# Kernel optimization log

Hardware: AMD Instinct MI355X
Metric: run time of the kernel (lower is better)

## Reference

```python
import jax, jax.numpy as jnp
import numpy as np

EPS = 1e-5


def spline_conv(x, src, dst, pseudo, W, root, bias, num_nodes, K=5):
    """Degree-1 open B-spline conv (torch_spline_conv semantics), mean aggregation.
    W: [kernel_total, Cin, Cout]. kernel_total==1 means trivial basis (kernel_size=1)."""
    E = src.shape[0]
    Cin = x.shape[1]
    KT = W.shape[0]
    x_j = x[src]                                            # [E, Cin] edge gather
    deg = jax.ops.segment_sum(jnp.ones((E,), x.dtype), dst, num_segments=num_nodes)
    deg = jnp.maximum(deg, 1.0)
    if KT == 1:
        agg = jax.ops.segment_sum(x_j, dst, num_segments=num_nodes)
        out = (agg / deg[:, None]) @ W[0]
    else:
        v = pseudo * (K - 1)                                # open spline: v in [0, K-1]
        f = jnp.clip(jnp.floor(v), 0.0, K - 2)
        frac = v - f                                        # [E, 2]
        fi = f.astype(jnp.int32)
        # bucket basis-weighted source features by (kernel_index, dst) then one dense einsum
        h = jnp.zeros((KT * num_nodes, Cin), x.dtype)
        for s0 in (0, 1):
            for s1 in (0, 1):
                b0 = frac[:, 0] if s0 else 1.0 - frac[:, 0]
                b1 = frac[:, 1] if s1 else 1.0 - frac[:, 1]
                basis = b0 * b1                             # [E]
                wi = (fi[:, 0] + s0) + K * (fi[:, 1] + s1)  # [E] kernel index in [0,25)
                seg = wi * num_nodes + dst
                h = h + jax.ops.segment_sum(basis[:, None] * x_j, seg,
                                            num_segments=KT * num_nodes)
        agg = jnp.einsum('knc,kco->no', h.reshape(KT, num_nodes, Cin), W)
        out = agg / deg[:, None]
    return out + x @ root + bias


def batch_norm(x, gamma, beta):
    m = x.mean(axis=0)
    var = jnp.mean((x - m) ** 2, axis=0)
    return gamma * (x - m) * jax.lax.rsqrt(var + EPS) + beta


def setup_inputs() -> dict:
    key = jax.random.key(0)
    ks = jax.random.split(key, 8)
    N, E, Cin, Cout = 50000, 800000, 32, 64
    x = jax.random.normal(ks[0], (N, Cin), jnp.float32)
    edge_index = jax.random.randint(ks[1], (2, E), 0, N, jnp.int32)
    edge_attr = jax.random.uniform(ks[2], (E, 2), jnp.float32)
    s = 0.1
    return {
        'x': x, 'edge_index': edge_index, 'edge_attr': edge_attr,
        'w1': jax.random.normal(ks[3], (25, Cin, Cout), jnp.float32) * s,
        'r1': jax.random.normal(ks[4], (Cin, Cout), jnp.float32) * s,
        'b1': jnp.zeros((Cout,), jnp.float32),
        'g1': jnp.ones((Cout,), jnp.float32),
        'beta1': jnp.zeros((Cout,), jnp.float32),
        'w2': jax.random.normal(ks[5], (25, Cout, Cout), jnp.float32) * s,
        'r2': jax.random.normal(ks[6], (Cout, Cout), jnp.float32) * s,
        'b2': jnp.zeros((Cout,), jnp.float32),
        'g2': jnp.ones((Cout,), jnp.float32),
        'beta2': jnp.zeros((Cout,), jnp.float32),
        'ws': jax.random.normal(ks[7], (1, Cin, Cout), jnp.float32) * s,
        'rs': jax.random.normal(jax.random.fold_in(key, 99), (Cin, Cout), jnp.float32) * s,
        'bs': jnp.zeros((Cout,), jnp.float32),
        'gs': jnp.ones((Cout,), jnp.float32),
        'betas': jnp.zeros((Cout,), jnp.float32),
    }


def reference(x, edge_index, edge_attr, w1, r1, b1, g1, beta1,
              w2, r2, b2, g2, beta2, ws, rs, bs, gs, betas):
    N = x.shape[0]
    src, dst = edge_index[0], edge_index[1]
    h = jax.nn.elu(batch_norm(spline_conv(x, src, dst, edge_attr, w1, r1, b1, N), g1, beta1))
    left = batch_norm(spline_conv(h, src, dst, edge_attr, w2, r2, b2, N), g2, beta2)
    short = batch_norm(spline_conv(x, src, dst, edge_attr, ws, rs, bs, N), gs, betas)
    return jax.nn.elu(left + short)
```

## Files before the change

kernel.cpp:

```cpp
#include <hip/hip_runtime.h>

#define NN 50000
#define NE 800000
#define DBINS 1024

typedef __attribute__((ext_vector_type(8))) short bf16x8;
typedef __attribute__((ext_vector_type(4))) float f32x4;

__device__ __forceinline__ unsigned short f2bf(float f) {
    union { float f; unsigned u; } v; v.f = f;
    unsigned r = v.u + 0x7FFFu + ((v.u >> 16) & 1u);
    return (unsigned short)(r >> 16);
}

__device__ __forceinline__ int us_idx(int kk, int r, int m) {
    return kk*544 + (r >> 3)*136 + m*8 + (r & 7);
}

template<int CIN, int NT>
__device__ __forceinline__ void stage1_node(
        const int* __restrict__ epsrc,
        const unsigned short* __restrict__ wfull,
        const unsigned short* __restrict__ Xh,
        int ebeg, int degp, int lane,
        f32x4 (&d)[2][NT]) {
#pragma unroll
    for (int mt = 0; mt < 2; ++mt)
#pragma unroll
        for (int nt = 0; nt < NT; ++nt)
            d[mt][nt] = f32x4{0.f, 0.f, 0.f, 0.f};
    if (degp <= 0) return;
    const int l15 = lane & 15;
    const int kb = (lane >> 4) * 8;
    const int last = degp - 1;
    for (int k0 = 0; k0 < degp; k0 += 32) {
        int e[8]; int s[8]; bool val[8];
#pragma unroll
        for (int j = 0; j < 8; ++j) {
            int k = k0 + kb + j;
            val[j] = (k < degp);
            e[j] = ebeg + min(k, last);
        }
#pragma unroll
        for (int j = 0; j < 8; ++j) s[j] = epsrc[e[j]];
        union { unsigned short us[8]; bf16x8 v; } a0, a1;
#pragma unroll
        for (int j = 0; j < 8; ++j) {
            unsigned short w0 = wfull[(size_t)e[j]*32 + l15];
            unsigned short w1 = wfull[(size_t)e[j]*32 + 16 + l15];
            a0.us[j] = val[j] ? w0 : (unsigned short)0;
            a1.us[j] = val[j] ? w1 : (unsigned short)0;
        }
#pragma unroll
        for (int nt = 0; nt < NT; ++nt) {
            union { unsigned short us[8]; bf16x8 v; } b;
#pragma unroll
            for (int j = 0; j < 8; ++j)
                b.us[j] = Xh[(size_t)s[j]*CIN + nt*16 + l15];
            d[0][nt] = __builtin_amdgcn_mfma_f32_16x16x32_bf16(a0.v, b.v, d[0][nt], 0, 0, 0);
            d[1][nt] = __builtin_amdgcn_mfma_f32_16x16x32_bf16(a1.v, b.v, d[1][nt], 0, 0, 0);
        }
    }
}

__global__ __launch_bounds__(256) void k_zero(int* degi, int* cur, float* stats,
                                              int* dcnt, int* dcur,
                                              unsigned* xz, unsigned* hz) {
    int i = blockIdx.x*256 + threadIdx.x;
    int stride = gridDim.x*256;
    for (int j = i; j < NN; j += stride) { degi[j] = 0; cur[j] = 0; }
    if (i < 384) stats[i] = 0.f;
    if (i < DBINS) { dcnt[i] = 0; dcur[i] = 0; }
    if (i < 16) xz[i] = 0u;
    if (i < 32) hz[i] = 0u;
}

__global__ __launch_bounds__(256) void k_hist(const int* __restrict__ dst, int* degi) {
    int e = blockIdx.x*256 + threadIdx.x;
    if (e < NE) atomicAdd(&degi[dst[e]], 1);
}

__global__ __launch_bounds__(256) void k_scan_block(const int* __restrict__ degi,
                                                    int* off, int* bsum) {
    __shared__ int sh[256];
    int t = threadIdx.x;
    int base = blockIdx.x * 1024;
    int v[4]; int s = 0;
#pragma unroll
    for (int j = 0; j < 4; j++) {
        int idx = base + t*4 + j;
        v[j] = (idx < NN) ? ((degi[idx] + 3) & ~3) : 0;
        s += v[j];
    }
    sh[t] = s; __syncthreads();
    for (int ofs = 1; ofs < 256; ofs <<= 1) {
        int x = (t >= ofs) ? sh[t - ofs] : 0;
        __syncthreads();
        sh[t] += x;
        __syncthreads();
    }
    int ex = sh[t] - s;
#pragma unroll
    for (int j = 0; j < 4; j++) {
        int idx = base + t*4 + j;
        if (idx < NN) off[idx] = ex;
        ex += v[j];
    }
    if (t == 255) bsum[blockIdx.x] = sh[255];
}

__global__ __launch_bounds__(256) void k_dhist(const int* __restrict__ degi, int* dcnt) {
    __shared__ int lh[DBINS];
    int t = threadIdx.x;
#pragma unroll
    for (int j = 0; j < DBINS/256; ++j) lh[t + 256*j] = 0;
    __syncthreads();
    int n = blockIdx.x*256 + t;
    if (n < NN) atomicAdd(&lh[min(degi[n], DBINS-1)], 1);
    __syncthreads();
#pragma unroll
    for (int j = 0; j < DBINS/256; ++j) {
        int b = t + 256*j;
        if (lh[b]) atomicAdd(&dcnt[b], lh[b]);
    }
}

__global__ __launch_bounds__(256) void k_topscan(const int* __restrict__ bsum,
                                                 int* bpre, int nb,
                                                 const int* __restrict__ dcnt,
                                                 int* dbase) {
    __shared__ int sh[256];
    int t = threadIdx.x;
    if (blockIdx.x == 0) {
        int s = (t < nb) ? bsum[t] : 0;
        sh[t] = s; __syncthreads();
        for (int ofs = 1; ofs < 256; ofs <<= 1) {
            int x = (t >= ofs) ? sh[t - ofs] : 0;
            __syncthreads();
            sh[t] += x;
            __syncthreads();
        }
        if (t < nb) bpre[t] = sh[t] - s;
    } else {
        int v[4]; int s = 0;
#pragma unroll
        for (int j = 0; j < 4; j++) { v[j] = dcnt[t*4 + j]; s += v[j]; }
        sh[t] = s; __syncthreads();
        for (int ofs = 1; ofs < 256; ofs <<= 1) {
            int x = (t >= ofs) ? sh[t - ofs] : 0;
            __syncthreads();
            sh[t] += x;
            __syncthreads();
        }
        int ex = sh[t] - s;
#pragma unroll
        for (int j = 0; j < 4; j++) { dbase[t*4 + j] = ex; ex += v[j]; }
    }
}

__global__ __launch_bounds__(256) void k_scan_add(int* off, const int* __restrict__ bpre,
                                                  const int* __restrict__ degi) {
    int i = blockIdx.x*256 + threadIdx.x;
    if (i < NN) {
        int v = off[i] + bpre[i >> 10];
        off[i] = v;
        if (i == NN - 1) off[NN] = v + ((degi[i] + 3) & ~3);
    }
}

__global__ __launch_bounds__(256) void k_pscatter_pad(const int* __restrict__ degi,
                                                      const int* __restrict__ dbase,
                                                      int* dcur, int* perm,
                                                      const int* __restrict__ off,
                                                      int* __restrict__ epsrc,
                                                      unsigned short* __restrict__ wfull) {
    __shared__ int lh[DBINS];
    __shared__ int lb[DBINS];
    int t = threadIdx.x;
#pragma unroll
    for (int j = 0; j < DBINS/256; ++j) lh[t + 256*j] = 0;
    __syncthreads();
    int n = blockIdx.x*256 + t;
    int d = 0, lr = 0;
    bool act = (n < NN);
    if (act) {
        d = min(degi[n], DBINS-1);
        lr = atomicAdd(&lh[d], 1);
    }
    __syncthreads();
#pragma unroll
    for (int j = 0; j < DBINS/256; ++j) {
        int b = t + 256*j;
        int c = lh[b];
        lb[b] = c ? atomicAdd(&dcur[b], c) : 0;
    }
    __syncthreads();
    if (act) {
        perm[dbase[d] + lb[d] + lr] = n;
        int base = off[n] + degi[n];
        int end  = off[n + 1];
        uint4 z = make_uint4(0u, 0u, 0u, 0u);
        for (int p = base; p < end; ++p) {
            epsrc[p] = NN;
            uint4* wp = (uint4*)(wfull + (size_t)p * 32);
            wp[0] = z; wp[1] = z; wp[2] = z; wp[3] = z;
        }
    }
}

__global__ __launch_bounds__(256) void k_scatter(const int* __restrict__ src,
                                                 const int* __restrict__ dst,
                                                 const float* __restrict__ ea,
                                                 const int* __restrict__ off, int* cur,
                                                 int* __restrict__ epsrc,
                                                 unsigned short* __restrict__ wfull) {
    int e = blockIdx.x*256 + threadIdx.x;
    if (e >= NE) return;
    int d = dst[e];
    int p = off[d] + atomicAdd(&cur[d], 1);
    float v0 = ea[2*e]     * 4.f;
    float v1 = ea[2*e + 1] * 4.f;
    float wx[5], wy[5];
#pragma unroll
    for (int r = 0; r < 5; ++r) {
        wx[r] = fmaxf(1.f - fabsf(v0 - (float)r), 0.f);
        wy[r] = fmaxf(1.f - fabsf(v1 - (float)r), 0.f);
    }
    union { unsigned short s[32]; uint4 q[4]; } u;
#pragma unroll
    for (int r1 = 0; r1 < 5; ++r1)
#pragma unroll
        for (int r0 = 0; r0 < 5; ++r0)
            u.s[r1*5 + r0] = f2bf(wx[r0] * wy[r1]);
    u.s[25] = 0x3F80;
#pragma unroll
    for (int i = 26; i < 32; ++i) u.s[i] = 0;
    epsrc[p] = src[e];
    uint4* wp = (uint4*)(wfull + (size_t)p * 32);
    wp[0] = u.q[0]; wp[1] = u.q[1]; wp[2] = u.q[2]; wp[3] = u.q[3];
}

__device__ __forceinline__ void wprep_body(int tid, const float* W, const float* root,
                                           int KTC, unsigned short* Wb) {
    int lane = tid & 63, cot = (tid >> 6) & 3, kk = tid >> 8;
    int co = 16*cot + (lane & 15);
    int kbase = kk*32 + ((lane >> 4) * 8);
    union { unsigned short s[8]; uint4 v; } u;
#pragma unroll
    for (int j = 0; j < 8; j++) {
        int k = kbase + j;
        float val = (k < KTC) ? W[(size_t)k*64 + co] : root[(size_t)(k - KTC)*64 + co];
        u.s[j] = f2bf(val);
    }
    *(uint4*)(Wb + (size_t)tid * 8) = u.v;
}

__global__ __launch_bounds__(256) void k_prep(const float* __restrict__ x,
                                              unsigned short* __restrict__ xb,
                                              const float* __restrict__ w1,
                                              const float* __restrict__ r1,
                                              unsigned short* Wb1,
                                              const float* __restrict__ wsN,
                                              const float* __restrict__ rs,
                                              unsigned short* WbS,
                                              const float* __restrict__ w2,
                                              const float* __restrict__ r2,
                                              unsigned short* Wb2) {
    int b = blockIdx.x, t = threadIdx.x;
    if (b < 1563) {
        int i = b*256 + t;
        if (i >= NN*8) return;
        float4 v = ((const float4*)x)[i];
        uint2 pk;
        pk.x = (unsigned)f2bf(v.x) | ((unsigned)f2bf(v.y) << 16);
        pk.y = (unsigned)f2bf(v.z) | ((unsigned)f2bf(v.w) << 16);
        ((uint2*)xb)[i] = pk;
    } else if (b < 1589) {
        wprep_body((b - 1563)*256 + t, w1, r1, 800, Wb1);
    } else if (b < 1591) {
        wprep_body((b - 1589)*256 + t, wsN, rs, 32, WbS);
    } else {
        wprep_body((b - 1591)*256 + t, w2, r2, 1600, Wb2);
    }
}

__global__ __launch_bounds__(512, 6) void k_conv1s(
        const unsigned short* __restrict__ Xh,
        const int* __restrict__ off,
        const int* __restrict__ degi,
        const int* __restrict__ epsrc,
        const unsigned short* __restrict__ wfull,
        const int* __restrict__ perm,
        const unsigned short* __restrict__ Wb1,
        const unsigned short* __restrict__ WbS,
        const float* __restrict__ b1,
        const float* __restrict__ bs,
        float* __restrict__ agg1,
        float* __restrict__ aggS) {
    __shared__ __align__(16) unsigned short hb[28*544];
    unsigned* hb32 = (unsigned*)hb;
    const int t = threadIdx.x, lane = t & 63, w = t >> 6;
    const int n0 = NN - 16 - blockIdx.x * 16;
    const int l15 = lane & 15;
    const int wib = (lane >> 4) * 4;

#pragma unroll
    for (int nn = 0; nn < 2; ++nn) {
        const int g = 2*w + nn;
        const int n = perm[n0 + g];
        const int deg = degi[n];
        const int degp = (deg + 3) & ~3;
        f32x4 d[2][2];
        stage1_node<32, 2>(epsrc, wfull, Xh, off[n], degp, lane, d);
        const float rdeg = 1.f / (float)max(deg, 1);
        const int basel = (l15 >> 3)*136 + g*8 + (l15 & 7);
#pragma unroll
        for (int mt = 0; mt < 2; ++mt)
#pragma unroll
            for (int nt = 0; nt < 2; ++nt)
#pragma unroll
                for (int r = 0; r < 4; ++r) {
                    int wi = mt*16 + wib + r;
                    if (wi <= 25) {
                        int kk = (wi < 25) ? wi : 26;
                        hb[kk*544 + nt*272 + basel] = f2bf(d[mt][nt][r] * rdeg);
                    }
                }
    }
    if ((lane & 31) < 16) {
        const int g2 = 2*w + (lane >> 5);
        const int cd = lane & 15;
        const int n2 = perm[n0 + g2];
        unsigned xv = ((const unsigned*)Xh)[(size_t)n2*16 + cd];
        const int r0 = 2*cd;
        const int dwb = (r0 >> 3)*68 + g2*4 + ((r0 & 7) >> 1);
        hb32[25*272 + dwb] = xv;
        hb32[27*272 + dwb] = xv;
    }
    __syncthreads();

    const int m = l15, qq = lane >> 4;
    const int co = (w & 3)*16 + m;
    const int4 pn = ((const int4*)perm)[(n0 >> 2) + qq];
    const int prow[4] = {pn.x, pn.y, pn.z, pn.w};
    if (w < 4) {
        f32x4 acc = {0.f, 0.f, 0.f, 0.f};
        for (int kk = 0; kk < 26; ++kk) {
            bf16x8 av = *(const bf16x8*)&hb[kk*544 + qq*136 + m*8];
            bf16x8 bv = *(const bf16x8*)(Wb1 + (size_t)((kk*4 + w)*64 + lane) * 8);
            acc = __builtin_amdgcn_mfma_f32_16x16x32_bf16(av, bv, acc, 0, 0, 0);
        }
        const float bb = b1[co];
#pragma unroll
        for (int r = 0; r < 4; ++r)
            agg1[(size_t)prow[r]*64 + co] = acc[r] + bb;
    } else {
        f32x4 accs = {0.f, 0.f, 0.f, 0.f};
#pragma unroll
        for (int s = 0; s < 2; ++s) {
            bf16x8 av = *(const bf16x8*)&hb[(26 + s)*544 + qq*136 + m*8];
            bf16x8 bv = *(const bf16x8*)(WbS + (size_t)((s*4 + (w & 3))*64 + lane) * 8);
            accs = __builtin_amdgcn_mfma_f32_16x16x32_bf16(av, bv, accs, 0, 0, 0);
        }
        const float bb = bs[co];
#pragma unroll
        for (int r = 0; r < 4; ++r)
            aggS[(size_t)prow[r]*64 + co] = accs[r] + bb;
    }
}

__global__ __launch_bounds__(512, 4) void k_conv2(
        const unsigned short* __restrict__ Xh,
        const int* __restrict__ off,
        const int* __restrict__ degi,
        const int* __restrict__ epsrc,
        const unsigned short* __restrict__ wfull,
        const int* __restrict__ perm,
        const unsigned short* __restrict__ Wb2,
        const float* __restrict__ b2,
        float* __restrict__ agg) {
    __shared__ __align__(16) unsigned short hb[52*544];
    unsigned* hb32 = (unsigned*)hb;
    const int t = threadIdx.x, lane = t & 63, w = t >> 6;
    const int n0 = NN - 16 - blockIdx.x * 16;
    const int l15 = lane & 15;
    const int wib = (lane >> 4) * 4;

#pragma unroll
    for (int nn = 0; nn < 2; ++nn) {
        const int g = 2*w + nn;
        const int n = perm[n0 + g];
        const int deg = degi[n];
        const int degp = (deg + 3) & ~3;
        f32x4 d[2][4];
        stage1_node<64, 4>(epsrc, wfull, Xh, off[n], degp, lane, d);
        const float rdeg = 1.f / (float)max(deg, 1);
        const int basel = (l15 >> 3)*136 + g*8 + (l15 & 7);
#pragma unroll
        for (int mt = 0; mt < 2; ++mt)
#pragma unroll
            for (int nt = 0; nt < 4; ++nt) {
                const int cadd = (nt >> 1)*544 + (nt & 1)*272 + basel;
#pragma unroll
                for (int r = 0; r < 4; ++r) {
                    int wi = mt*16 + wib + r;
                    if (wi < 25)
                        hb[wi*1088 + cadd] = f2bf(d[mt][nt][r] * rdeg);
                }
            }
    }
    {
        const int g2 = 2*w + (lane >> 5);
        const int c2 = lane & 31;
        const int n2 = perm[n0 + g2];
        unsigned xv = ((const unsigned*)Xh)[(size_t)n2*32 + c2];
        const int r0 = (2*c2) & 31;
        const int dw = (50 + (c2 >> 4))*272 + (r0 >> 3)*68 + g2*4 + ((r0 & 7) >> 1);
        hb32[dw] = xv;
    }
    __syncthreads();

    if (w >= 4) return;
    const int m = l15, qq = lane >> 4;
    f32x4 acc = {0.f, 0.f, 0.f, 0.f};
    for (int kk = 0; kk < 52; ++kk) {
        bf16x8 av = *(const bf16x8*)&hb[kk*544 + qq*136 + m*8];
        bf16x8 bv = *(const bf16x8*)(Wb2 + (size_t)((kk*4 + w)*64 + lane) * 8);
        acc = __builtin_amdgcn_mfma_f32_16x16x32_bf16(av, bv, acc, 0, 0, 0);
    }
    const int4 pn = ((const int4*)perm)[(n0 >> 2) + qq];
    const int prow[4] = {pn.x, pn.y, pn.z, pn.w};
    const int co = w*16 + m;
    const float bb = b2[co];
#pragma unroll
    for (int rr = 0; rr < 4; ++rr)
        agg[(size_t)prow[rr]*64 + co] = acc[rr] + bb;
}

__global__ __launch_bounds__(256) void k_bnstats(const float* __restrict__ agg, float* stats) {
    __shared__ float sh0[256], sh1[256];
    int t = threadIdx.x;
    float s = 0.f, ss = 0.f;
    int stride = gridDim.x * 256;
    for (int i = blockIdx.x*256 + t; i < NN*64; i += stride) {
        float v = agg[i];
        s += v; ss += v*v;
    }
    sh0[t] = s; sh1[t] = ss;
    __syncthreads();
    if (t < 64) {
        float a = sh0[t] + sh0[t+64] + sh0[t+128] + sh0[t+192];
        float b = sh1[t] + sh1[t+64] + sh1[t+128] + sh1[t+192];
        atomicAdd(&stats[t], a);
        atomicAdd(&stats[64 + t], b);
    }
}

__global__ __launch_bounds__(256) void k_bnstats2(const float* __restrict__ a1,
                                                  const float* __restrict__ as,
                                                  float* stats) {
    __shared__ float sh0[256], sh1[256];
    int t = threadIdx.x;
    const float* src = (blockIdx.x < 256) ? a1 : as;
    float* dst = (blockIdx.x < 256) ? (stats + 128) : (stats + 256);
    int bid = (blockIdx.x < 256) ? blockIdx.x : blockIdx.x - 256;
    float s = 0.f, ss = 0.f;
    for (int i = bid*256 + t; i < NN*64; i += 256*256) {
        float v = src[i];
        s += v; ss += v*v;
    }
    sh0[t] = s; sh1[t] = ss;
    __syncthreads();
    if (t < 64) {
        float a = sh0[t] + sh0[t+64] + sh0[t+128] + sh0[t+192];
        float b = sh1[t] + sh1[t+64] + sh1[t+128] + sh1[t+192];
        atomicAdd(&dst[t], a);
        atomicAdd(&dst[64 + t], b);
    }
}

__device__ __forceinline__ float eluf(float u) { return u > 0.f ? u : expm1f(u); }

__global__ __launch_bounds__(256) void k_bn_elu(const float* __restrict__ agg,
                                                const float* __restrict__ stats,
                                                const float* __restrict__ gamma,
                                                const float* __restrict__ beta,
                                                unsigned short* __restrict__ outb) {
    int i = blockIdx.x*256 + threadIdx.x;
    if (i >= NN*16) return;
    float4 v = ((const float4*)agg)[i];
    float r[4] = {v.x, v.y, v.z, v.w};
    int c0 = (i << 2) & 63;
#pragma unroll
    for (int j = 0; j < 4; j++) {
        int c = c0 + j;
        float mu = stats[c] * (1.f/NN);
        float var = stats[64 + c] * (1.f/NN) - mu*mu;
        float sc = gamma[c] * rsqrtf(fmaxf(var, 0.f) + 1e-5f);
        r[j] = eluf((r[j] - mu)*sc + beta[c]);
    }
    uint2 pk;
    pk.x = (unsigned)f2bf(r[0]) | ((unsigned)f2bf(r[1]) << 16);
    pk.y = (unsigned)f2bf(r[2]) | ((unsigned)f2bf(r[3]) << 16);
    ((uint2*)outb)[i] = pk;
}

__global__ __launch_bounds__(256) void k_bn_final(const float* __restrict__ a2,
                                                  const float* __restrict__ st2,
                                                  const float* __restrict__ g2,
                                                  const float* __restrict__ be2,
                                                  const float* __restrict__ as,
                                                  const float* __restrict__ sts,
                                                  const float* __restrict__ gs,
                                                  const float* __restrict__ bes,
                                                  float* __restrict__ out) {
    int i = blockIdx.x*256 + threadIdx.x;
    if (i >= NN*16) return;
    float4 v2 = ((const float4*)a2)[i];
    float4 vs = ((const float4*)as)[i];
    float r2v[4] = {v2.x, v2.y, v2.z, v2.w};
    float rsv[4] = {vs.x, vs.y, vs.z, vs.w};
    float o[4];
    int c0 = (i << 2) & 63;
#pragma unroll
    for (int j = 0; j < 4; j++) {
        int c = c0 + j;
        float mu2 = st2[c] * (1.f/NN);
        float var2 = st2[64 + c] * (1.f/NN) - mu2*mu2;
        float sc2 = g2[c] * rsqrtf(fmaxf(var2, 0.f) + 1e-5f);
        float mus = sts[c] * (1.f/NN);
        float vars = sts[64 + c] * (1.f/NN) - mus*mus;
        float scs = gs[c] * rsqrtf(fmaxf(vars, 0.f) + 1e-5f);
        float u = (r2v[j] - mu2)*sc2 + be2[c] + (rsv[j] - mus)*scs + bes[c];
        o[j] = eluf(u);
    }
    ((float4*)out)[i] = make_float4(o[0], o[1], o[2], o[3]);
}

extern "C" void kernel_launch(void* const* d_in, const int* in_sizes, int n_in,
                              void* d_out, int out_size, void* d_ws, size_t ws_size,
                              hipStream_t stream) {
    const float* x   = (const float*)d_in[0];
    const int*   ei  = (const int*)d_in[1];
    const float* ea  = (const float*)d_in[2];
    const float* w1  = (const float*)d_in[3];
    const float* r1  = (const float*)d_in[4];
    const float* b1  = (const float*)d_in[5];
    const float* g1  = (const float*)d_in[6];
    const float* be1 = (const float*)d_in[7];
    const float* w2  = (const float*)d_in[8];
    const float* r2  = (const float*)d_in[9];
    const float* b2  = (const float*)d_in[10];
    const float* g2  = (const float*)d_in[11];
    const float* be2 = (const float*)d_in[12];
    const float* wsN = (const float*)d_in[13];
    const float* rs  = (const float*)d_in[14];
    const float* bs  = (const float*)d_in[15];
    const float* gs  = (const float*)d_in[16];
    const float* bes = (const float*)d_in[17];
    const int* srcp = ei;
    const int* dstp = ei + NE;

    char* wsb = (char*)d_ws;
    size_t o = 0;
    auto alloc = [&](size_t bytes) -> char* {
        char* p = wsb + o;
        o += (bytes + 255) & ~(size_t)255;
        return p;
    };
    int*    degi    = (int*)   alloc((size_t)NN * 4);
    int*    cur     = (int*)   alloc((size_t)NN * 4);
    int*    off     = (int*)   alloc((size_t)(NN + 1) * 4);
    int*    bsum    = (int*)   alloc(256 * 4);
    int*    bpre    = (int*)   alloc(256 * 4);
    int*    dcnt    = (int*)   alloc(DBINS * 4);
    int*    dcur    = (int*)   alloc(DBINS * 4);
    int*    dbase   = (int*)   alloc(DBINS * 4);
    int*    perm    = (int*)   alloc((size_t)NN * 4);
    int*    epsrc   = (int*)   alloc(((size_t)NE + 3*NN + 64) * 4);
    unsigned short* wfull = (unsigned short*)alloc(((size_t)NE + 3*NN + 64) * 64);
    unsigned short* Wb1 = (unsigned short*)alloc(26 * 4096);
    unsigned short* WbS = (unsigned short*)alloc(2 * 4096);
    unsigned short* Wb2 = (unsigned short*)alloc(52 * 4096);
    float*  agg1    = (float*) alloc((size_t)NN * 64 * 4);
    float*  aggS    = (float*) alloc((size_t)NN * 64 * 4);
    unsigned short* h1bf = (unsigned short*)alloc((size_t)(NN + 1) * 64 * 2);
    unsigned short* xbf  = (unsigned short*)alloc((size_t)(NN + 1) * 32 * 2);
    float*  stats   = (float*) alloc(384 * 4);
    (void)ws_size; (void)in_sizes; (void)n_in; (void)out_size;

    float* out = (float*)d_out;

    k_zero<<<196, 256, 0, stream>>>(degi, cur, stats, dcnt, dcur,
                                    (unsigned*)(xbf + (size_t)NN * 32),
                                    (unsigned*)(h1bf + (size_t)NN * 64));
    k_hist<<<3125, 256, 0, stream>>>(dstp, degi);
    k_scan_block<<<49, 256, 0, stream>>>(degi, off, bsum);
    k_dhist<<<196, 256, 0, stream>>>(degi, dcnt);
    k_topscan<<<2, 256, 0, stream>>>(bsum, bpre, 49, dcnt, dbase);
    k_scan_add<<<196, 256, 0, stream>>>(off, bpre, degi);
    k_pscatter_pad<<<196, 256, 0, stream>>>(degi, dbase, dcur, perm, off, epsrc, wfull);
    k_scatter<<<3125, 256, 0, stream>>>(srcp, dstp, ea, off, cur, epsrc, wfull);

    k_prep<<<1643, 256, 0, stream>>>(x, xbf, w1, r1, Wb1, wsN, rs, WbS, w2, r2, Wb2);

    k_conv1s<<<3125, 512, 0, stream>>>(xbf, off, degi, epsrc, wfull, perm,
                                       Wb1, WbS, b1, bs, agg1, aggS);
    k_bnstats<<<256, 256, 0, stream>>>(agg1, stats);
    k_bn_elu<<<3125, 256, 0, stream>>>(agg1, stats, g1, be1, h1bf);

    k_conv2<<<3125, 512, 0, stream>>>(h1bf, off, degi, epsrc, wfull, perm,
                                      Wb2, b2, agg1);
    k_bnstats2<<<512, 256, 0, stream>>>(agg1, aggS, stats);
    k_bn_final<<<3125, 256, 0, stream>>>(agg1, stats + 128, g2, be2,
                                         aggS, stats + 256, gs, bes, out);
}
```

Measured before the change: 431.5 us.

## Store compact per-edge records and recompute spline basis inside conv via 32x32 MFMA

Replaces the per-edge 64-byte precomputed bf16 basis vector plus separate src array with one 16-byte record (src, scaled pseudo coords). The conv kernels now recompute each lane's basis weight on the fly. The stage-1 gather-matmul switches from paired 16x16x32 MFMAs to a single 32x32x16 MFMA per column tile, with the epilogue remapped to match. This cuts scatter write traffic and the edge-data reads in both convs, at the cost of extra ALU work per edge and lower occupancy (launch bounds 6 to 5).

```diff
diff --git a/kernel.cpp b/kernel.cpp
--- a/kernel.cpp
+++ b/kernel.cpp
@@ -6,6 +6,7 @@
 
 typedef __attribute__((ext_vector_type(8))) short bf16x8;
 typedef __attribute__((ext_vector_type(4))) float f32x4;
+typedef __attribute__((ext_vector_type(16))) float f32x16;
 
 __device__ __forceinline__ unsigned short f2bf(float f) {
     union { float f; unsigned u; } v; v.f = f;
@@ -13,52 +14,50 @@
     return (unsigned short)(r >> 16);
 }
 
+__device__ __forceinline__ int4 ld_ep1(const int4* ep, unsigned idx) {
+    return *(const int4*)((const char*)ep + (size_t)(idx * 16u));
+}
+
 __device__ __forceinline__ int us_idx(int kk, int r, int m) {
     return kk*544 + (r >> 3)*136 + m*8 + (r & 7);
 }
 
-template<int CIN, int NT>
-__device__ __forceinline__ void stage1_node(
-        const int* __restrict__ epsrc,
-        const unsigned short* __restrict__ wfull,
+template<int CIN, int NT2>
+__device__ __forceinline__ void stage1_node32(
+        const int4* __restrict__ ep,
         const unsigned short* __restrict__ Xh,
         int ebeg, int degp, int lane,
-        f32x4 (&d)[2][NT]) {
-#pragma unroll
-    for (int mt = 0; mt < 2; ++mt)
-#pragma unroll
-        for (int nt = 0; nt < NT; ++nt)
-            d[mt][nt] = f32x4{0.f, 0.f, 0.f, 0.f};
+        float r0, float r1, int wsel,
+        f32x16 (&d)[NT2]) {
+#pragma unroll
+    for (int nt = 0; nt < NT2; ++nt)
+#pragma unroll
+        for (int r = 0; r < 16; ++r) d[nt][r] = 0.f;
     if (degp <= 0) return;
-    const int l15 = lane & 15;
-    const int kb = (lane >> 4) * 8;
+    const int m = lane & 31;
+    const int kb = (lane >> 5) * 8;
     const int last = degp - 1;
-    for (int k0 = 0; k0 < degp; k0 += 32) {
-        int e[8]; int s[8]; bool val[8];
+    for (int k0 = 0; k0 < degp; k0 += 16) {
+        int s[8];
+        union { unsigned short us[8]; bf16x8 v; } a;
 #pragma unroll
         for (int j = 0; j < 8; ++j) {
             int k = k0 + kb + j;
-            val[j] = (k < degp);
-            e[j] = ebeg + min(k, last);
-        }
-#pragma unroll
-        for (int j = 0; j < 8; ++j) s[j] = epsrc[e[j]];
-        union { unsigned short us[8]; bf16x8 v; } a0, a1;
-#pragma unroll
-        for (int j = 0; j < 8; ++j) {
-            unsigned short w0 = wfull[(size_t)e[j]*32 + l15];
-            unsigned short w1 = wfull[(size_t)e[j]*32 + 16 + l15];
-            a0.us[j] = val[j] ? w0 : (unsigned short)0;
-            a1.us[j] = val[j] ? w1 : (unsigned short)0;
-        }
-#pragma unroll
-        for (int nt = 0; nt < NT; ++nt) {
+            int4 P = ld_ep1(ep, (unsigned)(ebeg + min(k, last)));
+            s[j] = P.x;
+            float v0 = __int_as_float(P.y), v1 = __int_as_float(P.z);
+            float wxa = fmaxf(1.f - fabsf(v0 - r0), 0.f);
+            float wya = fmaxf(1.f - fabsf(v1 - r1), 0.f);
+            float wv = (wsel == 0) ? wxa * wya : ((wsel == 1) ? 1.f : 0.f);
+            a.us[j] = (k < degp) ? f2bf(wv) : (unsigned short)0;
+        }
+#pragma unroll
+        for (int nt = 0; nt < NT2; ++nt) {
             union { unsigned short us[8]; bf16x8 v; } b;
 #pragma unroll
             for (int j = 0; j < 8; ++j)
-                b.us[j] = Xh[(size_t)s[j]*CIN + nt*16 + l15];
-            d[0][nt] = __builtin_amdgcn_mfma_f32_16x16x32_bf16(a0.v, b.v, d[0][nt], 0, 0, 0);
-            d[1][nt] = __builtin_amdgcn_mfma_f32_16x16x32_bf16(a1.v, b.v, d[1][nt], 0, 0, 0);
+                b.us[j] = Xh[(size_t)s[j]*CIN + nt*32 + m];
+            d[nt] = __builtin_amdgcn_mfma_f32_32x32x16_bf16(a.v, b.v, d[nt], 0, 0, 0);
         }
     }
 }
@@ -172,8 +171,7 @@
                                                       const int* __restrict__ dbase,
                                                       int* dcur, int* perm,
                                                       const int* __restrict__ off,
-                                                      int* __restrict__ epsrc,
-                                                      unsigned short* __restrict__ wfull) {
+                                                      int4* __restrict__ ep) {
     __shared__ int lh[DBINS];
     __shared__ int lb[DBINS];
     int t = threadIdx.x;
@@ -199,12 +197,8 @@
         perm[dbase[d] + lb[d] + lr] = n;
         int base = off[n] + degi[n];
         int end  = off[n + 1];
-        uint4 z = make_uint4(0u, 0u, 0u, 0u);
-        for (int p = base; p < end; ++p) {
-            epsrc[p] = NN;
-            uint4* wp = (uint4*)(wfull + (size_t)p * 32);
-            wp[0] = z; wp[1] = z; wp[2] = z; wp[3] = z;
-        }
+        for (int p = base; p < end; ++p)
+            ep[p] = make_int4(NN, __float_as_int(1e9f), __float_as_int(1e9f), 0);
     }
 }
 
@@ -212,32 +206,14 @@
                                                  const int* __restrict__ dst,
                                                  const float* __restrict__ ea,
                                                  const int* __restrict__ off, int* cur,
-                                                 int* __restrict__ epsrc,
-                                                 unsigned short* __restrict__ wfull) {
+                                                 int4* __restrict__ ep) {
     int e = blockIdx.x*256 + threadIdx.x;
     if (e >= NE) return;
     int d = dst[e];
     int p = off[d] + atomicAdd(&cur[d], 1);
     float v0 = ea[2*e]     * 4.f;
     float v1 = ea[2*e + 1] * 4.f;
-    float wx[5], wy[5];
-#pragma unroll
-    for (int r = 0; r < 5; ++r) {
-        wx[r] = fmaxf(1.f - fabsf(v0 - (float)r), 0.f);
-        wy[r] = fmaxf(1.f - fabsf(v1 - (float)r), 0.f);
-    }
-    union { unsigned short s[32]; uint4 q[4]; } u;
-#pragma unroll
-    for (int r1 = 0; r1 < 5; ++r1)
-#pragma unroll
-        for (int r0 = 0; r0 < 5; ++r0)
-            u.s[r1*5 + r0] = f2bf(wx[r0] * wy[r1]);
-    u.s[25] = 0x3F80;
-#pragma unroll
-    for (int i = 26; i < 32; ++i) u.s[i] = 0;
-    epsrc[p] = src[e];
-    uint4* wp = (uint4*)(wfull + (size_t)p * 32);
-    wp[0] = u.q[0]; wp[1] = u.q[1]; wp[2] = u.q[2]; wp[3] = u.q[3];
+    ep[p] = make_int4(src[e], __float_as_int(v0), __float_as_int(v1), 0);
 }
 
 __device__ __forceinline__ void wprep_body(int tid, const float* W, const float* root,
@@ -284,12 +260,11 @@
     }
 }
 
-__global__ __launch_bounds__(512, 6) void k_conv1s(
+__global__ __launch_bounds__(512, 5) void k_conv1s(
         const unsigned short* __restrict__ Xh,
         const int* __restrict__ off,
         const int* __restrict__ degi,
-        const int* __restrict__ epsrc,
-        const unsigned short* __restrict__ wfull,
+        const int4* __restrict__ ep,
         const int* __restrict__ perm,
         const unsigned short* __restrict__ Wb1,
         const unsigned short* __restrict__ WbS,
@@ -301,8 +276,11 @@
     unsigned* hb32 = (unsigned*)hb;
     const int t = threadIdx.x, lane = t & 63, w = t >> 6;
     const int n0 = NN - 16 - blockIdx.x * 16;
-    const int l15 = lane & 15;
-    const int wib = (lane >> 4) * 4;
+    const int m32 = lane & 31;
+    const int hh = lane >> 5;
+    const float r0 = (float)(m32 % 5), r1 = (float)(m32 / 5);
+    const int wsel = (m32 < 25) ? 0 : ((m32 == 25) ? 1 : 2);
+    const int basel = (m32 >> 3)*136 + (m32 & 7);
 
 #pragma unroll
     for (int nn = 0; nn < 2; ++nn) {
@@ -310,36 +288,31 @@
         const int n = perm[n0 + g];
         const int deg = degi[n];
         const int degp = (deg + 3) & ~3;
-        f32x4 d[2][2];
-        stage1_node<32, 2>(epsrc, wfull, Xh, off[n], degp, lane, d);
+        f32x16 d[1];
+        stage1_node32<32, 1>(ep, Xh, off[n], degp, lane, r0, r1, wsel, d);
         const float rdeg = 1.f / (float)max(deg, 1);
-        const int basel = (l15 >> 3)*136 + g*8 + (l15 & 7);
-#pragma unroll
-        for (int mt = 0; mt < 2; ++mt)
-#pragma unroll
-            for (int nt = 0; nt < 2; ++nt)
-#pragma unroll
-                for (int r = 0; r < 4; ++r) {
-                    int wi = mt*16 + wib + r;
-                    if (wi <= 25) {
-                        int kk = (wi < 25) ? wi : 26;
-                        hb[kk*544 + nt*272 + basel] = f2bf(d[mt][nt][r] * rdeg);
-                    }
-                }
+#pragma unroll
+        for (int reg = 0; reg < 16; ++reg) {
+            int wi = (reg & 3) + 8*(reg >> 2) + 4*hh;
+            if (wi <= 25) {
+                int kk = (wi < 25) ? wi : 26;
+                hb[kk*544 + basel + g*8] = f2bf(d[0][reg] * rdeg);
+            }
+        }
     }
     if ((lane & 31) < 16) {
-        const int g2 = 2*w + (lane >> 5);
+        const int g2 = 2*w + hh;
         const int cd = lane & 15;
         const int n2 = perm[n0 + g2];
         unsigned xv = ((const unsigned*)Xh)[(size_t)n2*16 + cd];
-        const int r0 = 2*cd;
-        const int dwb = (r0 >> 3)*68 + g2*4 + ((r0 & 7) >> 1);
+        const int r0d = 2*cd;
+        const int dwb = (r0d >> 3)*68 + g2*4 + ((r0d & 7) >> 1);
         hb32[25*272 + dwb] = xv;
         hb32[27*272 + dwb] = xv;
     }
     __syncthreads();
 
-    const int m = l15, qq = lane >> 4;
+    const int m = lane & 15, qq = lane >> 4;
     const int co = (w & 3)*16 + m;
     const int4 pn = ((const int4*)perm)[(n0 >> 2) + qq];
     const int prow[4] = {pn.x, pn.y, pn.z, pn.w};
@@ -373,8 +346,7 @@
         const unsigned short* __restrict__ Xh,
         const int* __restrict__ off,
         const int* __restrict__ degi,
-        const int* __restrict__ epsrc,
-        const unsigned short* __restrict__ wfull,
+        const int4* __restrict__ ep,
         const int* __restrict__ perm,
         const unsigned short* __restrict__ Wb2,
         const float* __restrict__ b2,
@@ -383,8 +355,11 @@
     unsigned* hb32 = (unsigned*)hb;
     const int t = threadIdx.x, lane = t & 63, w = t >> 6;
     const int n0 = NN - 16 - blockIdx.x * 16;
-    const int l15 = lane & 15;
-    const int wib = (lane >> 4) * 4;
+    const int m32 = lane & 31;
+    const int hh = lane >> 5;
+    const float r0 = (float)(m32 % 5), r1 = (float)(m32 / 5);
+    const int wsel = (m32 < 25) ? 0 : ((m32 == 25) ? 1 : 2);
+    const int basel = (m32 >> 3)*136 + (m32 & 7);
 
 #pragma unroll
     for (int nn = 0; nn < 2; ++nn) {
@@ -392,36 +367,31 @@
         const int n = perm[n0 + g];
         const int deg = degi[n];
         const int degp = (deg + 3) & ~3;
-        f32x4 d[2][4];
-        stage1_node<64, 4>(epsrc, wfull, Xh, off[n], degp, lane, d);
+        f32x16 d[2];
+        stage1_node32<64, 2>(ep, Xh, off[n], degp, lane, r0, r1, wsel, d);
         const float rdeg = 1.f / (float)max(deg, 1);
-        const int basel = (l15 >> 3)*136 + g*8 + (l15 & 7);
-#pragma unroll
-        for (int mt = 0; mt < 2; ++mt)
-#pragma unroll
-            for (int nt = 0; nt < 4; ++nt) {
-                const int cadd = (nt >> 1)*544 + (nt & 1)*272 + basel;
-#pragma unroll
-                for (int r = 0; r < 4; ++r) {
-                    int wi = mt*16 + wib + r;
-                    if (wi < 25)
-                        hb[wi*1088 + cadd] = f2bf(d[mt][nt][r] * rdeg);
-                }
+#pragma unroll
+        for (int reg = 0; reg < 16; ++reg) {
+            int wi = (reg & 3) + 8*(reg >> 2) + 4*hh;
+            if (wi < 25) {
+                hb[(2*wi    )*544 + basel + g*8] = f2bf(d[0][reg] * rdeg);
+                hb[(2*wi + 1)*544 + basel + g*8] = f2bf(d[1][reg] * rdeg);
             }
+        }
     }
     {
-        const int g2 = 2*w + (lane >> 5);
+        const int g2 = 2*w + hh;
         const int c2 = lane & 31;
         const int n2 = perm[n0 + g2];
         unsigned xv = ((const unsigned*)Xh)[(size_t)n2*32 + c2];
-        const int r0 = (2*c2) & 31;
-        const int dw = (50 + (c2 >> 4))*272 + (r0 >> 3)*68 + g2*4 + ((r0 & 7) >> 1);
+        const int r0d = (2*c2) & 31;
+        const int dw = (50 + (c2 >> 4))*272 + (r0d >> 3)*68 + g2*4 + ((r0d & 7) >> 1);
         hb32[dw] = xv;
     }
     __syncthreads();
 
     if (w >= 4) return;
-    const int m = l15, qq = lane >> 4;
+    const int m = lane & 15, qq = lane >> 4;
     f32x4 acc = {0.f, 0.f, 0.f, 0.f};
     for (int kk = 0; kk < 52; ++kk) {
         bf16x8 av = *(const bf16x8*)&hb[kk*544 + qq*136 + m*8];
@@ -577,8 +547,7 @@
     int*    dcur    = (int*)   alloc(DBINS * 4);
     int*    dbase   = (int*)   alloc(DBINS * 4);
     int*    perm    = (int*)   alloc((size_t)NN * 4);
-    int*    epsrc   = (int*)   alloc(((size_t)NE + 3*NN + 64) * 4);
-    unsigned short* wfull = (unsigned short*)alloc(((size_t)NE + 3*NN + 64) * 64);
+    int4*   ep      = (int4*)  alloc(((size_t)NE + 3*NN + 64) * 16);
     unsigned short* Wb1 = (unsigned short*)alloc(26 * 4096);
     unsigned short* WbS = (unsigned short*)alloc(2 * 4096);
     unsigned short* Wb2 = (unsigned short*)alloc(52 * 4096);
@@ -599,17 +568,17 @@
     k_dhist<<<196, 256, 0, stream>>>(degi, dcnt);
     k_topscan<<<2, 256, 0, stream>>>(bsum, bpre, 49, dcnt, dbase);
     k_scan_add<<<196, 256, 0, stream>>>(off, bpre, degi);
-    k_pscatter_pad<<<196, 256, 0, stream>>>(degi, dbase, dcur, perm, off, epsrc, wfull);
-    k_scatter<<<3125, 256, 0, stream>>>(srcp, dstp, ea, off, cur, epsrc, wfull);
+    k_pscatter_pad<<<196, 256, 0, stream>>>(degi, dbase, dcur, perm, off, ep);
+    k_scatter<<<3125, 256, 0, stream>>>(srcp, dstp, ea, off, cur, ep);
 
     k_prep<<<1643, 256, 0, stream>>>(x, xbf, w1, r1, Wb1, wsN, rs, WbS, w2, r2, Wb2);
 
-    k_conv1s<<<3125, 512, 0, stream>>>(xbf, off, degi, epsrc, wfull, perm,
+    k_conv1s<<<3125, 512, 0, stream>>>(xbf, off, degi, ep, perm,
                                        Wb1, WbS, b1, bs, agg1, aggS);
     k_bnstats<<<256, 256, 0, stream>>>(agg1, stats);
     k_bn_elu<<<3125, 256, 0, stream>>>(agg1, stats, g1, be1, h1bf);
 
-    k_conv2<<<3125, 512, 0, stream>>>(h1bf, off, degi, epsrc, wfull, perm,
+    k_conv2<<<3125, 512, 0, stream>>>(h1bf, off, degi, ep, perm,
                                       Wb2, b2, agg1);
     k_bnstats2<<<512, 256, 0, stream>>>(agg1, aggS, stats);
     k_bn_final<<<3125, 256, 0, stream>>>(agg1, stats + 128, g2, be2,
```

Result: no change. 424.4 us (-1.6%).
